# Optimization experiments

Hardware: AMD Instinct MI355X
Metric: run time of the kernel (lower is better)

The kernel has to match this reference:

```python
import jax, jax.numpy as jnp
import numpy as np

N = 50000
E = 800000
D = 128
L = 3
BN_EPS = 1e-5


def _bn(h, gamma, beta, mean, var):
    # eval-mode BatchNorm1d using running stats
    return (h - mean) * (gamma * jax.lax.rsqrt(var + BN_EPS)) + beta


def setup_inputs() -> dict:
    key = jax.random.key(0)
    ks = jax.random.split(key, 8)
    x = jax.random.normal(ks[0], (N, D), dtype=jnp.float32)
    edge_index = jax.random.randint(ks[1], (2, E), 0, N, dtype=jnp.int32)
    s = 1.0 / np.sqrt(D)
    W1 = jax.random.uniform(ks[2], (L, D, D), jnp.float32, -s, s)
    b1 = jax.random.uniform(ks[3], (L, D), jnp.float32, -s, s)
    W2 = jax.random.uniform(ks[4], (L, D, D), jnp.float32, -s, s)
    b2 = jax.random.uniform(ks[5], (L, D), jnp.float32, -s, s)
    # BN params: [L, 2, D] -> (inner mlp BN, outer BN) gamma/beta; running mean/var
    g = jnp.ones((L, 2, D), jnp.float32)
    be = jnp.zeros((L, 2, D), jnp.float32)
    rm = jax.random.normal(ks[6], (L, 2, D), dtype=jnp.float32) * 0.1
    rv = jax.random.uniform(ks[7], (L, 2, D), jnp.float32, 0.5, 1.5)
    return {"x": x, "edge_index": edge_index, "W1": W1, "b1": b1, "W2": W2,
            "b2": b2, "g": g, "be": be, "rm": rm, "rv": rv}


def reference(x, edge_index, W1, b1, W2, b2, g, be, rm, rv):
    src, dst = edge_index[0], edge_index[1]
    h = x
    for i in range(L):
        # GINConv (eps=0): (1+eps)*h + sum over in-neighbors
        agg = jax.ops.segment_sum(h[src], dst, num_segments=N)
        h = h + agg
        # mlp: Linear -> BN -> ReLU -> Linear
        h = jnp.maximum(_bn(h @ W1[i] + b1[i], g[i, 0], be[i, 0], rm[i, 0], rv[i, 0]), 0.0)
        h = h @ W2[i] + b2[i]
        # outer BN + ReLU (dropout is identity in eval)
        h = jnp.maximum(_bn(h, g[i, 1], be[i, 1], rm[i, 1], rv[i, 1]), 0.0)
    return h
```

## Files before the change

kernel.cpp:

```cpp
#include <hip/hip_runtime.h>
#include <stdint.h>

#define NN 50000
#define NE 800000
#define DD 128
#define NL 3
#define NB_E 200
#define EPB 4000
#define NBK 196
#define MH (NBK*NB_E)
#define LSTR 136

typedef __attribute__((ext_vector_type(8))) short short8;
typedef __attribute__((ext_vector_type(4))) float f32x4;

__device__ __forceinline__ float b2f(unsigned short u){
  union { unsigned int i; float f; } v; v.i = ((unsigned int)u) << 16; return v.f;
}
__device__ __forceinline__ unsigned short f2b(float f){
  union { float f; unsigned int i; } v; v.f = f;
  unsigned int r = 0x7FFFu + ((v.i >> 16) & 1u);
  return (unsigned short)((v.i + r) >> 16);
}

__global__ __launch_bounds__(256) void k_hist(const int* __restrict__ dst,
                                              int* __restrict__ blkhist){
  __shared__ int h[NBK];
  int t = threadIdx.x, b = blockIdx.x;
  for (int i = t; i < NBK; i += 256) h[i] = 0;
  __syncthreads();
  int e0 = b * EPB;
  for (int i = t; i < EPB; i += 256){
    int d = dst[e0 + i];
    atomicAdd(&h[d >> 8], 1);
  }
  __syncthreads();
  for (int i = t; i < NBK; i += 256) blkhist[i * NB_E + b] = h[i];
}

__global__ void k_scanA(const int* __restrict__ in, int* __restrict__ out,
                        int* __restrict__ bsum, int n){
  __shared__ int s[256];
  int t = threadIdx.x, i = blockIdx.x * 256 + t;
  int v = (i < n) ? in[i] : 0;
  s[t] = v; __syncthreads();
  for (int d = 1; d < 256; d <<= 1){
    int x = (t >= d) ? s[t - d] : 0;
    __syncthreads();
    s[t] += x;
    __syncthreads();
  }
  if (i < n) out[i] = s[t] - v;
  if (t == 255) bsum[blockIdx.x] = s[255];
}

__global__ void k_scanB(int* __restrict__ bsum, int nblk){
  __shared__ int s[256];
  int t = threadIdx.x;
  int v = (t < nblk) ? bsum[t] : 0;
  s[t] = v; __syncthreads();
  for (int d = 1; d < 256; d <<= 1){
    int x = (t >= d) ? s[t - d] : 0;
    __syncthreads();
    s[t] += x;
    __syncthreads();
  }
  if (t < nblk) bsum[t] = s[t] - v;
}

__global__ void k_scanC(int* __restrict__ out, const int* __restrict__ bsum, int n){
  int i = blockIdx.x * 256 + threadIdx.x;
  if (i < n) out[i] += bsum[blockIdx.x];
}

__global__ __launch_bounds__(256) void k_bin(const int* __restrict__ src,
    const int* __restrict__ dst, const int* __restrict__ pos,
    unsigned int* __restrict__ binned){
  __shared__ int cur[NBK];
  int t = threadIdx.x, b = blockIdx.x;
  for (int i = t; i < NBK; i += 256) cur[i] = pos[i * NB_E + b];
  __syncthreads();
  int e0 = b * EPB;
  for (int i = t; i < EPB; i += 256){
    int d = dst[e0 + i];
    int s = src[e0 + i];
    int p = atomicAdd(&cur[d >> 8], 1);
    binned[p] = ((unsigned int)d << 16) | (unsigned int)s;
  }
}

__global__ __launch_bounds__(256) void k_csr(const unsigned int* __restrict__ binned,
    const int* __restrict__ pos, int* __restrict__ offs, int* __restrict__ counts,
    int* __restrict__ csr_src){
  __shared__ int h[256], ex[256], cur[256];
  int t = threadIdx.x, b = blockIdx.x;
  int r0 = pos[b * NB_E];
  int r1 = (b == NBK - 1) ? NE : pos[(b + 1) * NB_E];
  h[t] = 0; __syncthreads();
  for (int i = r0 + t; i < r1; i += 256){
    unsigned int pv = binned[i];
    atomicAdd(&h[(pv >> 16) & 255], 1);
  }
  __syncthreads();
  int v = h[t];
  ex[t] = v; __syncthreads();
  for (int d = 1; d < 256; d <<= 1){
    int x = (t >= d) ? ex[t - d] : 0;
    __syncthreads();
    ex[t] += x;
    __syncthreads();
  }
  int base = r0 + ex[t] - v;
  cur[t] = base;
  int gd = b * 256 + t;
  if (gd < NN){ offs[gd] = base; counts[gd] = v; }
  __syncthreads();
  for (int i = r0 + t; i < r1; i += 256){
    unsigned int pv = binned[i];
    int dl = (pv >> 16) & 255;
    int s = pv & 0xFFFF;
    int p = atomicAdd(&cur[dl], 1);
    csr_src[p] = s;
  }
}

__global__ void k_prep_w(const float* __restrict__ W1, const float* __restrict__ W2,
    unsigned short* __restrict__ Wthi, unsigned short* __restrict__ Wtlo){
  int idx = blockIdx.x * 256 + threadIdx.x;
  int mat = idx >> 14;
  int rem = idx & 16383;
  int k = rem >> 7, j = rem & 127;
  int layer = mat >> 1, which = mat & 1;
  const float* srcW = which ? W2 : W1;
  float w = srcW[layer * 16384 + k * DD + j];
  unsigned short hi = f2b(w);
  Wthi[mat * 16384 + j * DD + k] = hi;
  Wtlo[mat * 16384 + j * DD + k] = f2b(w - b2f(hi));
}

__global__ void k_prep_bn(const float* __restrict__ b1, const float* __restrict__ b2,
    const float* __restrict__ g, const float* __restrict__ be,
    const float* __restrict__ rm, const float* __restrict__ rv,
    float* __restrict__ sc, float* __restrict__ sh){
  int idx = blockIdx.x * 256 + threadIdx.x;
  if (idx >= NL * 2 * DD) return;
  int j = idx & 127;
  int w = (idx >> 7) & 1;
  int l = idx >> 8;
  int p = (l * 2 + w) * DD + j;
  float s = g[p] * rsqrtf(rv[p] + 1e-5f);
  float bias = w ? b2[l * DD + j] : b1[l * DD + j];
  sc[p] = s;
  sh[p] = fmaf(bias - rm[p], s, be[p]);
}

__global__ void k_cvt(const float* __restrict__ x,
    unsigned short* __restrict__ hi, unsigned short* __restrict__ lo){
  int i = blockIdx.x * 256 + threadIdx.x;
  float4 a = ((const float4*)x)[2 * i];
  float4 b = ((const float4*)x)[2 * i + 1];
  float v[8] = {a.x, a.y, a.z, a.w, b.x, b.y, b.z, b.w};
  short8 h8, l8;
  #pragma unroll
  for (int c = 0; c < 8; ++c){
    unsigned short h = f2b(v[c]);
    h8[c] = (short)h; l8[c] = (short)f2b(v[c] - b2f(h));
  }
  ((short8*)hi)[i] = h8;
  ((short8*)lo)[i] = l8;
}

__global__ __launch_bounds__(256, 8) void k_agg(
    const unsigned short* __restrict__ Shi, const unsigned short* __restrict__ Slo,
    const int* __restrict__ offs, const int* __restrict__ counts,
    const int* __restrict__ csr_src,
    unsigned short* __restrict__ Ahi, unsigned short* __restrict__ Alo){
  int t = blockIdx.x * 256 + threadIdx.x;
  int row = t >> 4;
  int l = t & 15;
  const short8* H = (const short8*)Shi;
  const short8* L = (const short8*)Slo;
  int idx = row * 16 + l;
  short8 s_h = H[idx]; short8 s_l = L[idx];
  float acc[8];
  #pragma unroll
  for (int i = 0; i < 8; ++i)
    acc[i] = b2f((unsigned short)s_h[i]) + b2f((unsigned short)s_l[i]);

  int e = offs[row];
  int end = e + counts[row];
  for (; e + 8 <= end; e += 8){
    int i0 = csr_src[e],   i1 = csr_src[e+1], i2 = csr_src[e+2], i3 = csr_src[e+3];
    int i4 = csr_src[e+4], i5 = csr_src[e+5], i6 = csr_src[e+6], i7 = csr_src[e+7];
    short8 g0 = H[i0*16+l], g1 = H[i1*16+l], g2 = H[i2*16+l], g3 = H[i3*16+l];
    short8 g4 = H[i4*16+l], g5 = H[i5*16+l], g6 = H[i6*16+l], g7 = H[i7*16+l];
    #pragma unroll
    for (int i = 0; i < 8; ++i){
      acc[i] += (b2f((unsigned short)g0[i]) + b2f((unsigned short)g1[i]))
              + (b2f((unsigned short)g2[i]) + b2f((unsigned short)g3[i]))
              + (b2f((unsigned short)g4[i]) + b2f((unsigned short)g5[i]))
              + (b2f((unsigned short)g6[i]) + b2f((unsigned short)g7[i]));
    }
  }
  for (; e < end; ++e){
    short8 g0 = H[csr_src[e]*16 + l];
    #pragma unroll
    for (int i = 0; i < 8; ++i) acc[i] += b2f((unsigned short)g0[i]);
  }

  short8 oh, ol;
  #pragma unroll
  for (int i = 0; i < 8; ++i){
    unsigned short h = f2b(acc[i]);
    oh[i] = (short)h; ol[i] = (short)f2b(acc[i] - b2f(h));
  }
  ((short8*)Ahi)[idx] = oh;
  ((short8*)Alo)[idx] = ol;
}

template<int LAST>
__global__ __launch_bounds__(256, 4) void k_mlp2(
    const unsigned short* __restrict__ Ahi, const unsigned short* __restrict__ Alo,
    const unsigned short* __restrict__ W1h, const unsigned short* __restrict__ W1l,
    const unsigned short* __restrict__ W2h, const unsigned short* __restrict__ W2l,
    const float* __restrict__ sc1, const float* __restrict__ sh1,
    const float* __restrict__ sc2, const float* __restrict__ sh2,
    unsigned short* __restrict__ Ohi, unsigned short* __restrict__ Olo,
    float* __restrict__ Of)
{
  __shared__ __align__(16) char smem[2 * 64 * LSTR * 2];
  unsigned short* Ahi_s = (unsigned short*)smem;
  unsigned short* Alo_s = Ahi_s + 64 * LSTR;

  int t = threadIdx.x;
  int base = blockIdx.x * 64;

  {
    const short8* AH = (const short8*)Ahi;
    const short8* AL = (const short8*)Alo;
    #pragma unroll
    for (int it = 0; it < 4; ++it){
      int idx = it * 256 + t;
      int rl = idx >> 4, ch = idx & 15;
      int rg = base + rl; if (rg > NN - 1) rg = NN - 1;
      *(short8*)&Ahi_s[rl * LSTR + ch * 8] = AH[rg * 16 + ch];
      *(short8*)&Alo_s[rl * LSTR + ch * 8] = AL[rg * 16 + ch];
    }
  }
  __syncthreads();

  int wave = t >> 6, lane = t & 63, l16 = lane & 15, q = lane >> 4;
  int r0w = (wave >> 1) * 32;
  int c0 = (wave & 1) * 64;
  const short8* B1H = (const short8*)W1h;
  const short8* B1L = (const short8*)W1l;
  const short8* B2H = (const short8*)W2h;
  const short8* B2L = (const short8*)W2l;

  f32x4 acc[2][4];
  #pragma unroll
  for (int rt = 0; rt < 2; ++rt)
    #pragma unroll
    for (int ct = 0; ct < 4; ++ct) acc[rt][ct] = (f32x4){0.f, 0.f, 0.f, 0.f};
  #pragma unroll
  for (int kc = 0; kc < 4; ++kc){
    short8 ah0 = *(const short8*)&Ahi_s[(r0w + l16) * LSTR + kc * 32 + q * 8];
    short8 al0 = *(const short8*)&Alo_s[(r0w + l16) * LSTR + kc * 32 + q * 8];
    short8 ah1 = *(const short8*)&Ahi_s[(r0w + 16 + l16) * LSTR + kc * 32 + q * 8];
    short8 al1 = *(const short8*)&Alo_s[(r0w + 16 + l16) * LSTR + kc * 32 + q * 8];
    #pragma unroll
    for (int ct = 0; ct < 4; ++ct){
      int wr = c0 + ct * 16 + l16;
      short8 bh = B1H[wr * 16 + kc * 4 + q];
      short8 bl = B1L[wr * 16 + kc * 4 + q];
      acc[0][ct] = __builtin_amdgcn_mfma_f32_16x16x32_bf16(ah0, bh, acc[0][ct], 0, 0, 0);
      acc[0][ct] = __builtin_amdgcn_mfma_f32_16x16x32_bf16(ah0, bl, acc[0][ct], 0, 0, 0);
      acc[0][ct] = __builtin_amdgcn_mfma_f32_16x16x32_bf16(al0, bh, acc[0][ct], 0, 0, 0);
      acc[1][ct] = __builtin_amdgcn_mfma_f32_16x16x32_bf16(ah1, bh, acc[1][ct], 0, 0, 0);
      acc[1][ct] = __builtin_amdgcn_mfma_f32_16x16x32_bf16(ah1, bl, acc[1][ct], 0, 0, 0);
      acc[1][ct] = __builtin_amdgcn_mfma_f32_16x16x32_bf16(al1, bh, acc[1][ct], 0, 0, 0);
    }
  }
  __syncthreads();

  #pragma unroll
  for (int rt = 0; rt < 2; ++rt)
    #pragma unroll
    for (int ct = 0; ct < 4; ++ct){
      int col = c0 + ct * 16 + l16;
      float s = sc1[col], b = sh1[col];
      #pragma unroll
      for (int r = 0; r < 4; ++r){
        int rl = r0w + rt * 16 + q * 4 + r;
        float v = fmaxf(fmaf(acc[rt][ct][r], s, b), 0.f);
        unsigned short h = f2b(v);
        Ahi_s[rl * LSTR + col] = h;
        Alo_s[rl * LSTR + col] = f2b(v - b2f(h));
      }
    }
  __syncthreads();

  f32x4 acc2[2][4];
  #pragma unroll
  for (int rt = 0; rt < 2; ++rt)
    #pragma unroll
    for (int ct = 0; ct < 4; ++ct) acc2[rt][ct] = (f32x4){0.f, 0.f, 0.f, 0.f};
  #pragma unroll
  for (int kc = 0; kc < 4; ++kc){
    short8 ah0 = *(const short8*)&Ahi_s[(r0w + l16) * LSTR + kc * 32 + q * 8];
    short8 al0 = *(const short8*)&Alo_s[(r0w + l16) * LSTR + kc * 32 + q * 8];
    short8 ah1 = *(const short8*)&Ahi_s[(r0w + 16 + l16) * LSTR + kc * 32 + q * 8];
    short8 al1 = *(const short8*)&Alo_s[(r0w + 16 + l16) * LSTR + kc * 32 + q * 8];
    #pragma unroll
    for (int ct = 0; ct < 4; ++ct){
      int wr = c0 + ct * 16 + l16;
      short8 bh = B2H[wr * 16 + kc * 4 + q];
      short8 bl = B2L[wr * 16 + kc * 4 + q];
      acc2[0][ct] = __builtin_amdgcn_mfma_f32_16x16x32_bf16(ah0, bh, acc2[0][ct], 0, 0, 0);
      acc2[0][ct] = __builtin_amdgcn_mfma_f32_16x16x32_bf16(ah0, bl, acc2[0][ct], 0, 0, 0);
      acc2[0][ct] = __builtin_amdgcn_mfma_f32_16x16x32_bf16(al0, bh, acc2[0][ct], 0, 0, 0);
      acc2[1][ct] = __builtin_amdgcn_mfma_f32_16x16x32_bf16(ah1, bh, acc2[1][ct], 0, 0, 0);
      acc2[1][ct] = __builtin_amdgcn_mfma_f32_16x16x32_bf16(ah1, bl, acc2[1][ct], 0, 0, 0);
      acc2[1][ct] = __builtin_amdgcn_mfma_f32_16x16x32_bf16(al1, bh, acc2[1][ct], 0, 0, 0);
    }
  }
  __syncthreads();

  if (!LAST){
    #pragma unroll
    for (int rt = 0; rt < 2; ++rt)
      #pragma unroll
      for (int ct = 0; ct < 4; ++ct){
        int col = c0 + ct * 16 + l16;
        float s = sc2[col], b = sh2[col];
        #pragma unroll
        for (int r = 0; r < 4; ++r){
          int rl = r0w + rt * 16 + q * 4 + r;
          float v = fmaxf(fmaf(acc2[rt][ct][r], s, b), 0.f);
          unsigned short h = f2b(v);
          Ahi_s[rl * LSTR + col] = h;
          Alo_s[rl * LSTR + col] = f2b(v - b2f(h));
        }
      }
    int rr = lane >> 3, ch = lane & 7;
    #pragma unroll
    for (int i = 0; i < 4; ++i){
      int rl = r0w + i * 8 + rr;
      int rg = base + rl;
      short8 vh = *(const short8*)&Ahi_s[rl * LSTR + c0 + ch * 8];
      short8 vl = *(const short8*)&Alo_s[rl * LSTR + c0 + ch * 8];
      if (rg < NN){
        *(short8*)&Ohi[rg * DD + c0 + ch * 8] = vh;
        *(short8*)&Olo[rg * DD + c0 + ch * 8] = vl;
      }
    }
  } else {
    float* Cf = (float*)smem;
    #pragma unroll
    for (int rt = 0; rt < 2; ++rt)
      #pragma unroll
      for (int ct = 0; ct < 4; ++ct){
        int col = c0 + ct * 16 + l16;
        float s = sc2[col], b = sh2[col];
        #pragma unroll
        for (int r = 0; r < 4; ++r){
          int rl = r0w + rt * 16 + q * 4 + r;
          Cf[rl * 132 + col] = fmaxf(fmaf(acc2[rt][ct][r], s, b), 0.f);
        }
      }
    int rr = lane >> 4, cf = (lane & 15) * 4;
    #pragma unroll
    for (int i = 0; i < 8; ++i){
      int rl = r0w + i * 4 + rr;
      int rg = base + rl;
      float4 v = *(const float4*)&Cf[rl * 132 + c0 + cf];
      if (rg < NN) *(float4*)&Of[rg * DD + c0 + cf] = v;
    }
  }
}

extern "C" void kernel_launch(void* const* d_in, const int* in_sizes, int n_in,
                              void* d_out, int out_size, void* d_ws, size_t ws_size,
                              hipStream_t stream) {
  const float* x  = (const float*)d_in[0];
  const int* ei   = (const int*)d_in[1];
  const float* W1 = (const float*)d_in[2];
  const float* b1 = (const float*)d_in[3];
  const float* W2 = (const float*)d_in[4];
  const float* b2 = (const float*)d_in[5];
  const float* g  = (const float*)d_in[6];
  const float* be = (const float*)d_in[7];
  const float* rm = (const float*)d_in[8];
  const float* rv = (const float*)d_in[9];

  const int* src = ei;
  const int* dst = ei + NE;

  char* w = (char*)d_ws;
  const size_t HB = (size_t)NN * DD * sizeof(unsigned short);
  unsigned short* S0hi = (unsigned short*)w; w += HB;
  unsigned short* S0lo = (unsigned short*)w; w += HB;
  unsigned short* S1hi = (unsigned short*)w; w += HB;
  unsigned short* S1lo = (unsigned short*)w; w += HB;
  unsigned short* Ahi  = (unsigned short*)w; w += HB;
  unsigned short* Alo  = (unsigned short*)w; w += HB;
  unsigned short* Wthi = (unsigned short*)w; w += 6 * 16384 * sizeof(unsigned short);
  unsigned short* Wtlo = (unsigned short*)w; w += 6 * 16384 * sizeof(unsigned short);
  float* scv = (float*)w; w += NL * 2 * DD * sizeof(float);
  float* shv = (float*)w; w += NL * 2 * DD * sizeof(float);
  int* counts  = (int*)w; w += 200192;
  int* offs    = (int*)w; w += 200192;
  int* blkhist = (int*)w; w += MH * sizeof(int);
  int* pos     = (int*)w; w += MH * sizeof(int);
  int* bsum    = (int*)w; w += 1024;
  unsigned int* binned = (unsigned int*)w; w += (size_t)NE * sizeof(unsigned int);
  int* csr_src = (int*)w; w += (size_t)NE * sizeof(int);

  const int SCAN_BLK = (MH + 255) / 256;
  k_hist<<<NB_E, 256, 0, stream>>>(dst, blkhist);
  k_scanA<<<SCAN_BLK, 256, 0, stream>>>(blkhist, pos, bsum, MH);
  k_scanB<<<1, 256, 0, stream>>>(bsum, SCAN_BLK);
  k_scanC<<<SCAN_BLK, 256, 0, stream>>>(pos, bsum, MH);
  k_bin<<<NB_E, 256, 0, stream>>>(src, dst, pos, binned);
  k_csr<<<NBK, 256, 0, stream>>>(binned, pos, offs, counts, csr_src);

  k_prep_w<<<384, 256, 0, stream>>>(W1, W2, Wthi, Wtlo);
  k_prep_bn<<<3, 256, 0, stream>>>(b1, b2, g, be, rm, rv, scv, shv);
  k_cvt<<<NN * DD / 8 / 256, 256, 0, stream>>>(x, S0hi, S0lo);

  const int AGG_BLOCKS = NN * 16 / 256;
  const int MLP_BLOCKS = (NN + 63) / 64;

  for (int i = 0; i < NL; ++i){
    const unsigned short* W1h = Wthi + (size_t)(i * 2 + 0) * 16384;
    const unsigned short* W1l = Wtlo + (size_t)(i * 2 + 0) * 16384;
    const unsigned short* W2h = Wthi + (size_t)(i * 2 + 1) * 16384;
    const unsigned short* W2l = Wtlo + (size_t)(i * 2 + 1) * 16384;
    const float* sc1 = scv + (size_t)(i * 2 + 0) * DD;
    const float* sh1 = shv + (size_t)(i * 2 + 0) * DD;
    const float* sc2 = scv + (size_t)(i * 2 + 1) * DD;
    const float* sh2 = shv + (size_t)(i * 2 + 1) * DD;

    const unsigned short* Ih = (i & 1) ? S1hi : S0hi;
    const unsigned short* Il = (i & 1) ? S1lo : S0lo;
    unsigned short* Oh = (i & 1) ? S0hi : S1hi;
    unsigned short* Ol = (i & 1) ? S0lo : S1lo;

    k_agg<<<AGG_BLOCKS, 256, 0, stream>>>(Ih, Il, offs, counts, csr_src, Ahi, Alo);

    if (i == NL - 1){
      k_mlp2<1><<<MLP_BLOCKS, 256, 0, stream>>>(Ahi, Alo,
          W1h, W1l, W2h, W2l, sc1, sh1, sc2, sh2,
          (unsigned short*)nullptr, (unsigned short*)nullptr, (float*)d_out);
    } else {
      k_mlp2<0><<<MLP_BLOCKS, 256, 0, stream>>>(Ahi, Alo,
          W1h, W1l, W2h, W2l, sc1, sh1, sc2, sh2, Oh, Ol, (float*)nullptr);
    }
  }
}
```

Before: 351.0 us.

## Load MLP A operand directly from global and use 2-wave 64x64 warp tiles

```diff
diff --git a/kernel.cpp b/kernel.cpp
--- a/kernel.cpp
+++ b/kernel.cpp
@@ -219,7 +219,7 @@
 }
 
 template<int LAST>
-__global__ __launch_bounds__(256, 4) void k_mlp2(
+__global__ __launch_bounds__(128, 2) void k_mlp3(
     const unsigned short* __restrict__ Ahi, const unsigned short* __restrict__ Alo,
     const unsigned short* __restrict__ W1h, const unsigned short* __restrict__ W1l,
     const unsigned short* __restrict__ W2h, const unsigned short* __restrict__ W2l,
@@ -229,126 +229,129 @@
     float* __restrict__ Of)
 {
   __shared__ __align__(16) char smem[2 * 64 * LSTR * 2];
-  unsigned short* Ahi_s = (unsigned short*)smem;
-  unsigned short* Alo_s = Ahi_s + 64 * LSTR;
+  unsigned short* Hhi_s = (unsigned short*)smem;
+  unsigned short* Hlo_s = Hhi_s + 64 * LSTR;
 
   int t = threadIdx.x;
   int base = blockIdx.x * 64;
-
-  {
-    const short8* AH = (const short8*)Ahi;
-    const short8* AL = (const short8*)Alo;
-    #pragma unroll
-    for (int it = 0; it < 4; ++it){
-      int idx = it * 256 + t;
-      int rl = idx >> 4, ch = idx & 15;
-      int rg = base + rl; if (rg > NN - 1) rg = NN - 1;
-      *(short8*)&Ahi_s[rl * LSTR + ch * 8] = AH[rg * 16 + ch];
-      *(short8*)&Alo_s[rl * LSTR + ch * 8] = AL[rg * 16 + ch];
-    }
-  }
-  __syncthreads();
-
   int wave = t >> 6, lane = t & 63, l16 = lane & 15, q = lane >> 4;
-  int r0w = (wave >> 1) * 32;
-  int c0 = (wave & 1) * 64;
+  int c0 = wave * 64;
+
+  const short8* AH = (const short8*)Ahi;
+  const short8* AL = (const short8*)Alo;
   const short8* B1H = (const short8*)W1h;
   const short8* B1L = (const short8*)W1l;
   const short8* B2H = (const short8*)W2h;
   const short8* B2L = (const short8*)W2l;
 
-  f32x4 acc[2][4];
-  #pragma unroll
-  for (int rt = 0; rt < 2; ++rt)
+  int ar[4];
+  #pragma unroll
+  for (int rt = 0; rt < 4; ++rt){
+    int r = base + rt * 16 + l16;
+    ar[rt] = (r > NN - 1) ? (NN - 1) : r;
+  }
+
+  f32x4 acc[4][4];
+  #pragma unroll
+  for (int rt = 0; rt < 4; ++rt)
     #pragma unroll
     for (int ct = 0; ct < 4; ++ct) acc[rt][ct] = (f32x4){0.f, 0.f, 0.f, 0.f};
+
   #pragma unroll
   for (int kc = 0; kc < 4; ++kc){
-    short8 ah0 = *(const short8*)&Ahi_s[(r0w + l16) * LSTR + kc * 32 + q * 8];
-    short8 al0 = *(const short8*)&Alo_s[(r0w + l16) * LSTR + kc * 32 + q * 8];
-    short8 ah1 = *(const short8*)&Ahi_s[(r0w + 16 + l16) * LSTR + kc * 32 + q * 8];
-    short8 al1 = *(const short8*)&Alo_s[(r0w + 16 + l16) * LSTR + kc * 32 + q * 8];
+    short8 ah[4], al[4], bh[4], bl[4];
+    #pragma unroll
+    for (int rt = 0; rt < 4; ++rt){
+      ah[rt] = AH[ar[rt] * 16 + kc * 4 + q];
+      al[rt] = AL[ar[rt] * 16 + kc * 4 + q];
+    }
     #pragma unroll
     for (int ct = 0; ct < 4; ++ct){
       int wr = c0 + ct * 16 + l16;
-      short8 bh = B1H[wr * 16 + kc * 4 + q];
-      short8 bl = B1L[wr * 16 + kc * 4 + q];
-      acc[0][ct] = __builtin_amdgcn_mfma_f32_16x16x32_bf16(ah0, bh, acc[0][ct], 0, 0, 0);
-      acc[0][ct] = __builtin_amdgcn_mfma_f32_16x16x32_bf16(ah0, bl, acc[0][ct], 0, 0, 0);
-      acc[0][ct] = __builtin_amdgcn_mfma_f32_16x16x32_bf16(al0, bh, acc[0][ct], 0, 0, 0);
-      acc[1][ct] = __builtin_amdgcn_mfma_f32_16x16x32_bf16(ah1, bh, acc[1][ct], 0, 0, 0);
-      acc[1][ct] = __builtin_amdgcn_mfma_f32_16x16x32_bf16(ah1, bl, acc[1][ct], 0, 0, 0);
-      acc[1][ct] = __builtin_amdgcn_mfma_f32_16x16x32_bf16(al1, bh, acc[1][ct], 0, 0, 0);
-    }
-  }
-  __syncthreads();
-
-  #pragma unroll
-  for (int rt = 0; rt < 2; ++rt)
+      bh[ct] = B1H[wr * 16 + kc * 4 + q];
+      bl[ct] = B1L[wr * 16 + kc * 4 + q];
+    }
+    #pragma unroll
+    for (int rt = 0; rt < 4; ++rt)
+      #pragma unroll
+      for (int ct = 0; ct < 4; ++ct){
+        acc[rt][ct] = __builtin_amdgcn_mfma_f32_16x16x32_bf16(ah[rt], bh[ct], acc[rt][ct], 0, 0, 0);
+        acc[rt][ct] = __builtin_amdgcn_mfma_f32_16x16x32_bf16(ah[rt], bl[ct], acc[rt][ct], 0, 0, 0);
+        acc[rt][ct] = __builtin_amdgcn_mfma_f32_16x16x32_bf16(al[rt], bh[ct], acc[rt][ct], 0, 0, 0);
+      }
+  }
+
+  #pragma unroll
+  for (int ct = 0; ct < 4; ++ct){
+    int col = c0 + ct * 16 + l16;
+    float s = sc1[col], b = sh1[col];
+    #pragma unroll
+    for (int rt = 0; rt < 4; ++rt)
+      #pragma unroll
+      for (int r = 0; r < 4; ++r){
+        int rl = rt * 16 + q * 4 + r;
+        float v = fmaxf(fmaf(acc[rt][ct][r], s, b), 0.f);
+        unsigned short h = f2b(v);
+        Hhi_s[rl * LSTR + col] = h;
+        Hlo_s[rl * LSTR + col] = f2b(v - b2f(h));
+      }
+  }
+  __syncthreads();
+
+  f32x4 acc2[4][4];
+  #pragma unroll
+  for (int rt = 0; rt < 4; ++rt)
+    #pragma unroll
+    for (int ct = 0; ct < 4; ++ct) acc2[rt][ct] = (f32x4){0.f, 0.f, 0.f, 0.f};
+
+  #pragma unroll
+  for (int kc = 0; kc < 4; ++kc){
+    short8 ah[4], al[4], bh[4], bl[4];
+    #pragma unroll
+    for (int rt = 0; rt < 4; ++rt){
+      ah[rt] = *(const short8*)&Hhi_s[(rt * 16 + l16) * LSTR + kc * 32 + q * 8];
+      al[rt] = *(const short8*)&Hlo_s[(rt * 16 + l16) * LSTR + kc * 32 + q * 8];
+    }
+    #pragma unroll
+    for (int ct = 0; ct < 4; ++ct){
+      int wr = c0 + ct * 16 + l16;
+      bh[ct] = B2H[wr * 16 + kc * 4 + q];
+      bl[ct] = B2L[wr * 16 + kc * 4 + q];
+    }
+    #pragma unroll
+    for (int rt = 0; rt < 4; ++rt)
+      #pragma unroll
+      for (int ct = 0; ct < 4; ++ct){
+        acc2[rt][ct] = __builtin_amdgcn_mfma_f32_16x16x32_bf16(ah[rt], bh[ct], acc2[rt][ct], 0, 0, 0);
+        acc2[rt][ct] = __builtin_amdgcn_mfma_f32_16x16x32_bf16(ah[rt], bl[ct], acc2[rt][ct], 0, 0, 0);
+        acc2[rt][ct] = __builtin_amdgcn_mfma_f32_16x16x32_bf16(al[rt], bh[ct], acc2[rt][ct], 0, 0, 0);
+      }
+  }
+  __syncthreads();
+
+  if (!LAST){
     #pragma unroll
     for (int ct = 0; ct < 4; ++ct){
       int col = c0 + ct * 16 + l16;
-      float s = sc1[col], b = sh1[col];
+      float s = sc2[col], b = sh2[col];
       #pragma unroll
-      for (int r = 0; r < 4; ++r){
-        int rl = r0w + rt * 16 + q * 4 + r;
-        float v = fmaxf(fmaf(acc[rt][ct][r], s, b), 0.f);
-        unsigned short h = f2b(v);
-        Ahi_s[rl * LSTR + col] = h;
-        Alo_s[rl * LSTR + col] = f2b(v - b2f(h));
-      }
-    }
-  __syncthreads();
-
-  f32x4 acc2[2][4];
-  #pragma unroll
-  for (int rt = 0; rt < 2; ++rt)
-    #pragma unroll
-    for (int ct = 0; ct < 4; ++ct) acc2[rt][ct] = (f32x4){0.f, 0.f, 0.f, 0.f};
-  #pragma unroll
-  for (int kc = 0; kc < 4; ++kc){
-    short8 ah0 = *(const short8*)&Ahi_s[(r0w + l16) * LSTR + kc * 32 + q * 8];
-    short8 al0 = *(const short8*)&Alo_s[(r0w + l16) * LSTR + kc * 32 + q * 8];
-    short8 ah1 = *(const short8*)&Ahi_s[(r0w + 16 + l16) * LSTR + kc * 32 + q * 8];
-    short8 al1 = *(const short8*)&Alo_s[(r0w + 16 + l16) * LSTR + kc * 32 + q * 8];
-    #pragma unroll
-    for (int ct = 0; ct < 4; ++ct){
-      int wr = c0 + ct * 16 + l16;
-      short8 bh = B2H[wr * 16 + kc * 4 + q];
-      short8 bl = B2L[wr * 16 + kc * 4 + q];
-      acc2[0][ct] = __builtin_amdgcn_mfma_f32_16x16x32_bf16(ah0, bh, acc2[0][ct], 0, 0, 0);
-      acc2[0][ct] = __builtin_amdgcn_mfma_f32_16x16x32_bf16(ah0, bl, acc2[0][ct], 0, 0, 0);
-      acc2[0][ct] = __builtin_amdgcn_mfma_f32_16x16x32_bf16(al0, bh, acc2[0][ct], 0, 0, 0);
-      acc2[1][ct] = __builtin_amdgcn_mfma_f32_16x16x32_bf16(ah1, bh, acc2[1][ct], 0, 0, 0);
-      acc2[1][ct] = __builtin_amdgcn_mfma_f32_16x16x32_bf16(ah1, bl, acc2[1][ct], 0, 0, 0);
-      acc2[1][ct] = __builtin_amdgcn_mfma_f32_16x16x32_bf16(al1, bh, acc2[1][ct], 0, 0, 0);
-    }
-  }
-  __syncthreads();
-
-  if (!LAST){
-    #pragma unroll
-    for (int rt = 0; rt < 2; ++rt)
-      #pragma unroll
-      for (int ct = 0; ct < 4; ++ct){
-        int col = c0 + ct * 16 + l16;
-        float s = sc2[col], b = sh2[col];
+      for (int rt = 0; rt < 4; ++rt)
         #pragma unroll
         for (int r = 0; r < 4; ++r){
-          int rl = r0w + rt * 16 + q * 4 + r;
+          int rl = rt * 16 + q * 4 + r;
           float v = fmaxf(fmaf(acc2[rt][ct][r], s, b), 0.f);
           unsigned short h = f2b(v);
-          Ahi_s[rl * LSTR + col] = h;
-          Alo_s[rl * LSTR + col] = f2b(v - b2f(h));
+          Hhi_s[rl * LSTR + col] = h;
+          Hlo_s[rl * LSTR + col] = f2b(v - b2f(h));
         }
-      }
+    }
     int rr = lane >> 3, ch = lane & 7;
     #pragma unroll
-    for (int i = 0; i < 4; ++i){
-      int rl = r0w + i * 8 + rr;
+    for (int i = 0; i < 8; ++i){
+      int rl = i * 8 + rr;
       int rg = base + rl;
-      short8 vh = *(const short8*)&Ahi_s[rl * LSTR + c0 + ch * 8];
-      short8 vl = *(const short8*)&Alo_s[rl * LSTR + c0 + ch * 8];
+      short8 vh = *(const short8*)&Hhi_s[rl * LSTR + c0 + ch * 8];
+      short8 vl = *(const short8*)&Hlo_s[rl * LSTR + c0 + ch * 8];
       if (rg < NN){
         *(short8*)&Ohi[rg * DD + c0 + ch * 8] = vh;
         *(short8*)&Olo[rg * DD + c0 + ch * 8] = vl;
@@ -357,21 +360,21 @@
   } else {
     float* Cf = (float*)smem;
     #pragma unroll
-    for (int rt = 0; rt < 2; ++rt)
+    for (int ct = 0; ct < 4; ++ct){
+      int col = c0 + ct * 16 + l16;
+      float s = sc2[col], b = sh2[col];
       #pragma unroll
-      for (int ct = 0; ct < 4; ++ct){
-        int col = c0 + ct * 16 + l16;
-        float s = sc2[col], b = sh2[col];
+      for (int rt = 0; rt < 4; ++rt)
         #pragma unroll
         for (int r = 0; r < 4; ++r){
-          int rl = r0w + rt * 16 + q * 4 + r;
+          int rl = rt * 16 + q * 4 + r;
           Cf[rl * 132 + col] = fmaxf(fmaf(acc2[rt][ct][r], s, b), 0.f);
         }
-      }
+    }
     int rr = lane >> 4, cf = (lane & 15) * 4;
     #pragma unroll
-    for (int i = 0; i < 8; ++i){
-      int rl = r0w + i * 4 + rr;
+    for (int i = 0; i < 16; ++i){
+      int rl = i * 4 + rr;
       int rg = base + rl;
       float4 v = *(const float4*)&Cf[rl * 132 + c0 + cf];
       if (rg < NN) *(float4*)&Of[rg * DD + c0 + cf] = v;
@@ -449,11 +452,11 @@
     k_agg<<<AGG_BLOCKS, 256, 0, stream>>>(Ih, Il, offs, counts, csr_src, Ahi, Alo);
 
     if (i == NL - 1){
-      k_mlp2<1><<<MLP_BLOCKS, 256, 0, stream>>>(Ahi, Alo,
+      k_mlp3<1><<<MLP_BLOCKS, 128, 0, stream>>>(Ahi, Alo,
           W1h, W1l, W2h, W2l, sc1, sh1, sc2, sh2,
           (unsigned short*)nullptr, (unsigned short*)nullptr, (float*)d_out);
     } else {
-      k_mlp2<0><<<MLP_BLOCKS, 256, 0, stream>>>(Ahi, Alo,
+      k_mlp3<0><<<MLP_BLOCKS, 128, 0, stream>>>(Ahi, Alo,
           W1h, W1l, W2h, W2l, sc1, sh1, sc2, sh2, Oh, Ol, (float*)nullptr);
     }
   }
```

New measurement: 319.6 us. -8.9%, faster.
